# Kernel tuning notes

Hardware: AMD Instinct MI355X
Metric: run time of the kernel (lower is better)

The kernel has to match this reference:

```python
import jax, jax.numpy as jnp
import numpy as np

# Physical constants and grid (match torch WRF.__init__)
PREF = 100000.0
RD = 287.0
G = 9.81
NX, NY, NZ = 384, 384, 48
DX, DY = 1000.0, 1000.0
DZ = 1.0 / (NZ + 1)

# --- staggered-grid stencil primitives (replace F.conv3d with shifts) ---

def pad_x(X):
    # periodic in x
    return jnp.concatenate([X[:, :, -1:], X, X[:, :, :1]], axis=2)

def pad_y(X):
    # periodic in y
    return jnp.concatenate([X[:, -1:, :], X, X[:, :1, :]], axis=1)

def pad_z(X, top=None, surface=None):
    # Dirichlet in z (defaults to zero boundary planes)
    top = top if top is not None else jnp.zeros_like(X[:1])
    surface = surface if surface is not None else jnp.zeros_like(X[:1])
    return jnp.concatenate([top, X, surface], axis=0)

def bar_x(X):
    return (X[:, :, 1:] + X[:, :, :-1]) * 0.5

def bar_y(X):
    return (X[:, 1:, :] + X[:, :-1, :]) * 0.5

def bar_z(X):
    return (X[1:] + X[:-1]) * 0.5

def delta_x(X):
    return (X[:, :, 1:] - X[:, :, :-1]) / DX

def delta_y(X):
    return (X[:, 1:, :] - X[:, :-1, :]) / DY

def delta_z(X):
    return (X[1:] - X[:-1]) / DZ


def rhs(U, V, W, Theta, Mu, Phi, Phi_t, Phi_s, P_t, P_s):
    u = U / bar_x(pad_x(Mu))                      # (NZ, NY, NX+1)
    v = V / bar_y(pad_y(Mu))                      # (NZ, NY+1, NX)
    w = W / bar_z(Mu)                             # (NZ-1, NY, NX)
    alpha = -delta_z(pad_z(Phi, Phi_t, Phi_s)) / Mu   # (NZ, NY, NX)
    theta = Theta / Mu
    p = PREF * (RD * theta / PREF / alpha) ** 1.4
    omega = -w * G / bar_z(alpha) / bar_z(Mu)     # (NZ-1, NY, NX)
    Omega = omega * bar_z(Mu)

    R_U = (-delta_x(bar_x(pad_x(U)) * bar_x(pad_x(u)))
           - delta_y(bar_x(pad_x(V)) * bar_y(pad_y(u)))
           - delta_z(bar_x(pad_x(pad_z(Omega))) * bar_z(pad_z(u))))
    R_V = (-delta_x(bar_y(pad_y(U)) * bar_x(pad_x(v)))
           - delta_y(bar_y(pad_y(V)) * bar_y(pad_y(v)))
           - delta_z(bar_y(pad_y(pad_z(Omega))) * bar_z(pad_z(v))))
    R_W = (-delta_x(bar_z(U) * bar_x(pad_x(w)))
           - delta_y(bar_z(V) * bar_y(pad_y(w)))
           - delta_z(bar_z(pad_z(Omega)) * bar_z(pad_z(w))))
    R_Theta = (-delta_x(U * bar_x(pad_x(theta)))
               - delta_y(V * bar_y(pad_y(theta)))
               - delta_z(pad_z(Omega) * bar_z(pad_z(theta))))
    R_Phi = (-bar_z(bar_x(u)) * delta_x(bar_x(pad_x(Phi)))
             - bar_z(bar_y(v)) * delta_y(bar_y(pad_y(Phi)))
             - omega * delta_z(bar_z(pad_z(Phi, Phi_t, Phi_s))))
    R_Mu = -delta_x(U) - delta_y(V) - delta_z(pad_z(Omega))

    # pressure-gradient terms
    R_U = R_U + (-bar_x(pad_x(Mu)) * bar_x(pad_x(alpha)) * delta_x(pad_x(p))
                 - delta_z(bar_x(bar_z(pad_x(pad_z(p, P_t, P_s)))))
                   * delta_x(pad_x(bar_z(pad_z(Phi, Phi_t, Phi_s)))))
    R_V = R_V + (-bar_y(pad_y(Mu)) * bar_y(pad_y(alpha)) * delta_y(pad_y(p))
                 - delta_z(bar_y(bar_z(pad_y(pad_z(p, P_t, P_s)))))
                   * delta_y(pad_y(bar_z(pad_z(Phi, Phi_t, Phi_s)))))
    R_W = R_W + G * (delta_z(p) - bar_z(Mu))
    R_Phi = R_Phi + G * w
    return R_U, R_V, R_W, R_Theta, R_Mu, R_Phi


def rk3_step(U, V, W, Theta, Mu, Phi, Phi_t, Phi_s, P_t, P_s, dt):
    Uc, Vc, Wc, Tc, Mc, Pc = U, V, W, Theta, Mu, Phi
    for c in (dt / 3.0, dt / 2.0, dt * 1.0):
        rU, rV, rW, rT, rM, rP = rhs(Uc, Vc, Wc, Tc, Mc, Pc, Phi_t, Phi_s, P_t, P_s)
        Uc = U + c * rU
        Vc = V + c * rV
        Wc = W + c * rW
        Tc = Theta + c * rT
        Mc = Mu + c * rM
        Pc = Phi + c * rP
    return (Uc, Vc, Wc, Tc, Mc, Pc)


def setup_inputs() -> dict:
    key = jax.random.key(0)
    k_th, k_u, k_v, k_w = jax.random.split(key, 4)
    # potential temperature with boundary layers, ~300 K
    theta_full = 300.0 + 0.5 * jax.random.normal(k_th, (NZ + 2, NY, NX), dtype=jnp.float32)
    P_t = jnp.zeros((1, NY, NX), dtype=jnp.float32)
    P_s = jnp.full((1, NY, NX), PREF, dtype=jnp.float32)
    # reproduce __init__ hydrostatic setup
    P = jnp.linspace(DZ, 1.0 - DZ, NZ, dtype=jnp.float32).reshape(NZ, 1, 1) * (P_s - P_t) + P_t
    Alpha = RD / PREF * theta_full[1:-1] * (P / PREF) ** (-1.0 / 1.4)
    Mu = jnp.broadcast_to(P_s - P_t, (NZ, NY, NX)).astype(jnp.float32)
    layer = Mu * Alpha * DZ                                  # (NZ, NY, NX)
    # Phi_full[i] = sum_{j>=i} layer[j], Phi_full[NZ] = 0
    Phi_full = jnp.concatenate(
        [jnp.flip(jnp.cumsum(jnp.flip(layer, 0), axis=0), 0),
         jnp.zeros((1, NY, NX), dtype=jnp.float32)], axis=0)  # (NZ+1, NY, NX)
    Phi_t = Phi_full[:1]
    Phi_s = Phi_full[-1:]
    Phi = Phi_full[1:-1]                                     # (NZ-1, NY, NX)
    Theta = theta_full[1:-1] * Mu
    U = 5e5 * jax.random.normal(k_u, (NZ, NY, NX + 1), dtype=jnp.float32)
    V = 5e5 * jax.random.normal(k_v, (NZ, NY + 1, NX), dtype=jnp.float32)
    W = 1e4 * jax.random.normal(k_w, (NZ - 1, NY, NX), dtype=jnp.float32)
    return {"U": U, "V": V, "W": W, "Theta": Theta, "Mu": Mu, "Phi": Phi,
            "Phi_t": Phi_t, "Phi_s": Phi_s, "P_t": P_t, "P_s": P_s, "dt": 4}


def reference(U, V, W, Theta, Mu, Phi, Phi_t, Phi_s, P_t, P_s, dt):
    return rk3_step(U, V, W, Theta, Mu, Phi, Phi_t, Phi_s, P_t, P_s, dt)
```

## Files before the change

kernel.cpp:

```cpp
#include <hip/hip_runtime.h>

namespace {

constexpr int NX = 384, NY = 384, NZ = 48;
constexpr int NXU = NX + 1;
constexpr int PLN = NX * NY;
constexpr float RDX = 1.0f / 1000.0f;
constexpr float RDY = 1.0f / 1000.0f;
constexpr float RDZ = 49.0f;
constexpr float PREF = 100000.0f, G = 9.81f;
constexpr float K_RP = 287.0f / PREF;

constexpr int SZ_U = NZ * NY * NXU;
constexpr int SZ_V = NZ * (NY + 1) * NX;
constexpr int SZ_W = (NZ - 1) * PLN;
constexpr int SZ_T = NZ * PLN;
constexpr int SZ_M = NZ * PLN;
constexpr int SZ_P = (NZ - 1) * PLN;

constexpr int TX = 32, TY = 8;
constexpr int PW = TX + 3;
constexpr int PH = TY + 3;
constexpr int PSZ = PW * PH;
constexpr int WW = PW + 1;
constexpr int WH = PH + 1;
constexpr int WSZ = WW * WH;
constexpr int ZP = 448;
constexpr int KCH = 12, KSPLIT = 4;

constexpr int GX = NX / TX;
constexpr int GY = NY / TY;
constexpr int NWG = GX * GY * KSPLIT;
constexpr int CPX = NWG / 8;

constexpr int O_PH = 0;
constexpr int O_MS = O_PH + 5 * ZP;
constexpr int O_UR = O_MS + 4 * ZP;
constexpr int O_VR = O_UR + 3 * ZP;
constexpr int O_TS = O_VR + 3 * ZP;
constexpr int O_WS = O_TS + ZP;
constexpr int O_P  = O_WS + ZP;
constexpr int O_OM = O_P  + 3 * PSZ;
constexpr int O_TH = O_OM + 3 * PSZ;
constexpr int O_u  = O_TH + 2 * PSZ;
constexpr int O_v  = O_u  + 2 * PSZ;
constexpr int O_w  = O_v  + 2 * PSZ;
constexpr int LTOT = O_w + 2 * PSZ;

struct PIdx { int pix, uo, vo, wc, oxa, oxb, oya, oyb; };

__device__ __forceinline__ float frcp(float x) { return __builtin_amdgcn_rcpf(x); }
__device__ __forceinline__ float pow14(float x) {
    return __builtin_amdgcn_exp2f(1.4f * __builtin_amdgcn_logf(x));
}
__device__ __forceinline__ void gll4(const float* src, float* ldsWaveBase) {
    __builtin_amdgcn_global_load_lds(
        (const __attribute__((address_space(1))) void*)src,
        (__attribute__((address_space(3))) void*)ldsWaveBase, 4, 0, 0);
}
__device__ __forceinline__ int imin(int a, int b) { return a < b ? a : b; }
__device__ __forceinline__ int imax(int a, int b) { return a > b ? a : b; }

__global__ __launch_bounds__(256, 3)
void rhs_tile(
    const float* __restrict__ Us, const float* __restrict__ Vs, const float* __restrict__ Ws,
    const float* __restrict__ Ts, const float* __restrict__ Ms, const float* __restrict__ Ps,
    const float* __restrict__ Phit, const float* __restrict__ Phis,
    const float* __restrict__ Pt,   const float* __restrict__ Psrf,
    const float* __restrict__ U0, const float* __restrict__ V0, const float* __restrict__ W0,
    const float* __restrict__ T0, const float* __restrict__ M0, const float* __restrict__ P0,
    float* __restrict__ Uo, float* __restrict__ Vo, float* __restrict__ Wo,
    float* __restrict__ To, float* __restrict__ Mo, float* __restrict__ Po,
    const int* __restrict__ dtp, float coef)
{
    __shared__ float L[LTOT];

    const int tx = threadIdx.x, ty = threadIdx.y;
    const int tid = ty * TX + tx;

    const int flat = blockIdx.x + GX * (blockIdx.y + GY * blockIdx.z);
    const int nf   = (flat & 7) * CPX + (flat >> 3);
    const int bx   = nf % GX;
    const int by   = (nf / GX) % GY;
    const int bz   = nf / (GX * GY);
    const int i0 = bx * TX;
    const int j0 = by * TY;
    const int k0 = bz * KCH;

    const int i = i0 + tx, j = j0 + ty;
    const float c = coef * (float)(*dtp);
    const int ly = ty + 1, lx = tx + 1;
    const int wb = tid & ~63;
    const bool w2 = (tid < 192);
    const bool hasB = (tid + 256 < PSZ);
    const bool hasW = (tid + 256 < WSZ);

    auto mkpt = [&](int idx, PIdx& q) {
        const int r = idx / PW, cc = idx - r * PW;
        int gj = j0 - 1 + r;  if (gj < 0) gj += NY; else if (gj >= NY) gj -= NY;
        int gi = i0 - 1 + cc; if (gi < 0) gi += NX; else if (gi >= NX) gi -= NX;
        int gII = i0 - 1 + cc; if (gII < 0) gII += NX + 1; else if (gII > NX) gII -= NX + 1;
        int gJJ = j0 - 1 + r;  if (gJJ < 0) gJJ += NY + 1; else if (gJJ > NY) gJJ -= NY + 1;
        q.pix = gj * NX + gi;
        q.uo  = gj * NXU + gII;
        q.vo  = gJJ * NX + gi;
        q.wc  = (r + 1) * WW + (cc + 1);
        q.oxa = q.wc - 1; q.oxb = q.wc;
        if (i0 == 0 && cc == 0) { q.oxa = q.wc; q.oxb = q.wc + 1; }
        q.oya = q.wc - WW; q.oyb = q.wc;
        if (j0 == 0 && r == 0)  { q.oya = q.wc; q.oyb = q.wc + WW; }
    };
    auto mkwide = [&](int idxw) -> int {
        const int r = idxw / WW, cc = idxw - r * WW;
        int gj = j0 - 2 + r;  if (gj < 0) gj += NY; else if (gj >= NY) gj -= NY;
        int gi = i0 - 2 + cc; if (gi < 0) gi += NX; else if (gi >= NX) gi -= NX;
        return gj * NX + gi;
    };
    PIdx A, B;
    mkpt(tid, A);
    mkpt(imin(tid + 256, PSZ - 1), B);
    const int pwA = mkwide(tid);
    const int pwB = mkwide(imin(tid + 256, WSZ - 1));

    auto stage = [&](int k) {
        {
            const int m = k + 3;
            const float* sA = (m >= NZ - 1) ? &Phis[A.pix] : &Ps[m * PLN + A.pix];
            gll4(sA, &L[O_PH + (m % 5) * ZP + wb]);
            if (w2) {
                const float* sB = (m >= NZ - 1) ? &Phis[B.pix] : &Ps[m * PLN + B.pix];
                gll4(sB, &L[O_PH + (m % 5) * ZP + wb + 256]);
            }
        }
        {
            const int lm = imin(k + 3, NZ - 1);
            gll4(&Ms[lm * PLN + pwA], &L[O_MS + ((k + 3) % 4) * ZP + wb]);
            if (w2) gll4(&Ms[lm * PLN + pwB], &L[O_MS + ((k + 3) % 4) * ZP + wb + 256]);
        }
        {
            const int lc = imin(k + 2, NZ - 1);
            gll4(&Us[lc * NY * NXU + A.uo], &L[O_UR + ((k + 2) % 3) * ZP + wb]);
            if (w2) gll4(&Us[lc * NY * NXU + B.uo], &L[O_UR + ((k + 2) % 3) * ZP + wb + 256]);
            gll4(&Vs[lc * (NY + 1) * NX + A.vo], &L[O_VR + ((k + 2) % 3) * ZP + wb]);
            if (w2) gll4(&Vs[lc * (NY + 1) * NX + B.vo], &L[O_VR + ((k + 2) % 3) * ZP + wb + 256]);
            gll4(&Ts[lc * PLN + A.pix], &L[O_TS + wb]);
            if (w2) gll4(&Ts[lc * PLN + B.pix], &L[O_TS + wb + 256]);
            const int lw = imin(k + 2, NZ - 2);
            gll4(&Ws[lw * PLN + A.pix], &L[O_WS + wb]);
            if (w2) gll4(&Ws[lw * PLN + B.pix], &L[O_WS + wb + 256]);
        }
    };

    auto derive = [&](int l, int idx, const PIdx& q, float tsv, float wsv) {
        const int s3 = ((l % 3) + 3) % 3, s2 = l & 1;
        float pv, th = 0.f, uv = 0.f, vv = 0.f, wv = 0.f, om = 0.f;
        if (l >= 0 && l < NZ) {
            const int m4 = l % 4, m5 = l % 5, p5 = ((l - 1) % 5 + 5) % 5;
            const float mu  = L[O_MS + m4 * ZP + q.wc];
            const float phv = L[O_PH + m5 * ZP + idx];
            const float phm = L[O_PH + p5 * ZP + idx];
            const float rmu = frcp(mu);
            const float al  = -(phv - phm) * RDZ * rmu;
            th = tsv * rmu;
            pv = PREF * pow14(K_RP * th * frcp(al));
            uv = L[O_UR + (l % 3) * ZP + idx]
                 * frcp(0.5f * (L[O_MS + m4 * ZP + q.oxa] + L[O_MS + m4 * ZP + q.oxb]));
            vv = L[O_VR + (l % 3) * ZP + idx]
                 * frcp(0.5f * (L[O_MS + m4 * ZP + q.oya] + L[O_MS + m4 * ZP + q.oyb]));
            if (l < NZ - 1) {
                const float mu1 = L[O_MS + ((l + 1) % 4) * ZP + q.wc];
                const float ph1 = L[O_PH + ((l + 1) % 5) * ZP + idx];
                const float al1 = -(ph1 - phv) * RDZ * frcp(mu1);
                const float mz  = 0.5f * (mu + mu1);
                wv = wsv * frcp(mz);
                om = -wsv * G * frcp(0.5f * (al + al1) * mz);
            }
        } else {
            pv = (l < 0) ? Pt[q.pix] : Psrf[q.pix];
        }
        L[O_P  + s3 * PSZ + idx] = pv;
        L[O_OM + s3 * PSZ + idx] = om;
        L[O_TH + s2 * PSZ + idx] = th;
        L[O_u  + s2 * PSZ + idx] = uv;
        L[O_v  + s2 * PSZ + idx] = vv;
        L[O_w  + s2 * PSZ + idx] = wv;
    };

    {
        for (int m = k0 - 2; m <= k0 + 2; ++m) {
            const float v = (m >= NZ - 1) ? Phis[A.pix]
                          : ((m < 0) ? Phit[A.pix] : Ps[m * PLN + A.pix]);
            L[O_PH + ((m % 5 + 5) % 5) * ZP + tid] = v;
        }
        for (int l = k0 - 1; l <= k0 + 2; ++l) {
            const int lc = imin(imax(l, 0), NZ - 1);
            L[O_MS + ((l % 4 + 4) % 4) * ZP + tid] = Ms[lc * PLN + pwA];
        }
        for (int l = k0 - 1; l <= k0 + 1; ++l) {
            const int lc = imin(imax(l, 0), NZ - 1);
            L[O_UR + ((l % 3 + 3) % 3) * ZP + tid] = Us[lc * NY * NXU + A.uo];
            L[O_VR + ((l % 3 + 3) % 3) * ZP + tid] = Vs[lc * (NY + 1) * NX + A.vo];
        }
        if (hasB) {
            const int idx = tid + 256;
            for (int m = k0 - 2; m <= k0 + 2; ++m) {
                const float v = (m >= NZ - 1) ? Phis[B.pix]
                              : ((m < 0) ? Phit[B.pix] : Ps[m * PLN + B.pix]);
                L[O_PH + ((m % 5 + 5) % 5) * ZP + idx] = v;
            }
            for (int l = k0 - 1; l <= k0 + 1; ++l) {
                const int lc = imin(imax(l, 0), NZ - 1);
                L[O_UR + ((l % 3 + 3) % 3) * ZP + idx] = Us[lc * NY * NXU + B.uo];
                L[O_VR + ((l % 3 + 3) % 3) * ZP + idx] = Vs[lc * (NY + 1) * NX + B.vo];
            }
        }
        if (hasW) {
            const int idx = tid + 256;
            for (int l = k0 - 1; l <= k0 + 2; ++l) {
                const int lc = imin(imax(l, 0), NZ - 1);
                L[O_MS + ((l % 4 + 4) % 4) * ZP + idx] = Ms[lc * PLN + pwB];
            }
        }
    }
    __syncthreads();

    {
        int lc = imin(imax(k0 - 1, 0), NZ - 1), lw = imin(imax(k0 - 1, 0), NZ - 2);
        derive(k0 - 1, tid, A, Ts[lc * PLN + A.pix], Ws[lw * PLN + A.pix]);
        if (hasB) derive(k0 - 1, tid + 256, B, Ts[lc * PLN + B.pix], Ws[lw * PLN + B.pix]);
        lc = imin(k0, NZ - 1); lw = imin(k0, NZ - 2);
        derive(k0, tid, A, Ts[lc * PLN + A.pix], Ws[lw * PLN + A.pix]);
        if (hasB) derive(k0, tid + 256, B, Ts[lc * PLN + B.pix], Ws[lw * PLN + B.pix]);
    }
    {
        const int lc = imin(k0 + 1, NZ - 1), lw = imin(k0 + 1, NZ - 2);
        gll4(&Ts[lc * PLN + A.pix], &L[O_TS + wb]);
        if (w2) gll4(&Ts[lc * PLN + B.pix], &L[O_TS + wb + 256]);
        gll4(&Ws[lw * PLN + A.pix], &L[O_WS + wb]);
        if (w2) gll4(&Ws[lw * PLN + B.pix], &L[O_WS + wb + 256]);
    }
    __syncthreads();

    const int e0 = (k0 - 1) & 1;
    float th_m  = L[O_TH + e0 * PSZ + ly * PW + lx];
    float u_m   = L[O_u  + e0 * PSZ + ly * PW + lx];
    float u_m_e = L[O_u  + e0 * PSZ + ly * PW + lx + 1];
    float v_m   = L[O_v  + e0 * PSZ + ly * PW + lx];
    float v_m_e = L[O_v  + e0 * PSZ + (ly + 1) * PW + lx];
    float w_m   = L[O_w  + e0 * PSZ + ly * PW + lx];

    for (int k = k0; k < k0 + KCH; ++k) {
        derive(k + 1, tid, A, L[O_TS + tid], L[O_WS + tid]);
        if (hasB) derive(k + 1, tid + 256, B, L[O_TS + tid + 256], L[O_WS + tid + 256]);
        __syncthreads();

        if (k < k0 + KCH - 1) stage(k);

        const int a5 = (k + 4) % 5, b5 = k % 5, c5 = (k + 1) % 5;
        const int aP = (k + 2) % 3, bP = k % 3, cP = (k + 1) % 3;
        const int m4 = k % 4, n4 = (k + 1) % 4;
        const int e = k & 1, f = 1 - e;
        const int eU = k % 3, fU = (k + 1) % 3;

        auto PHx = [&](int s, int rr, int cc) { return L[O_PH + s * ZP + rr * PW + cc]; };
        auto Px  = [&](int s, int rr, int cc) { return L[O_P  + s * PSZ + rr * PW + cc]; };
        auto Ox  = [&](int s, int rr, int cc) { return L[O_OM + s * PSZ + rr * PW + cc]; };
        auto MUx = [&](int s, int rr, int cc) { return L[O_MS + s * ZP + (rr + 1) * WW + cc + 1]; };
        auto THx = [&](int s, int rr, int cc) { return L[O_TH + s * PSZ + rr * PW + cc]; };
        auto URx = [&](int s, int rr, int cc) { return L[O_UR + s * ZP + rr * PW + cc]; };
        auto VRx = [&](int s, int rr, int cc) { return L[O_VR + s * ZP + rr * PW + cc]; };
        auto ux  = [&](int s, int rr, int cc) { return L[O_u  + s * PSZ + rr * PW + cc]; };
        auto vx  = [&](int s, int rr, int cc) { return L[O_v  + s * PSZ + rr * PW + cc]; };
        auto wx  = [&](int s, int rr, int cc) { return L[O_w  + s * PSZ + rr * PW + cc]; };
        auto ALk = [&](int rr, int cc) {
            return -(PHx(b5, rr, cc) - PHx(a5, rr, cc)) * RDZ * frcp(MUx(m4, rr, cc));
        };

        auto R_U_c = [&](int cc, float ukm) -> float {
            const float u0 = ux(e, ly, cc), um = ux(e, ly, cc - 1), up = ux(e, ly, cc + 1);
            const float Uc = URx(eU, ly, cc), Um = URx(eU, ly, cc - 1), Up = URx(eU, ly, cc + 1);
            float r = -0.25f * ((Uc + Up) * (u0 + up) - (Um + Uc) * (um + u0)) * RDX;
            const float VBj  = 0.5f * (VRx(eU, ly, cc - 1) + VRx(eU, ly, cc));
            const float VBj1 = 0.5f * (VRx(eU, ly + 1, cc - 1) + VRx(eU, ly + 1, cc));
            const float uS = ux(e, ly - 1, cc), uN = ux(e, ly + 1, cc);
            r -= (VBj1 * 0.5f * (u0 + uN) - VBj * 0.5f * (uS + u0)) * RDY;
            const float OBk  = 0.5f * (Ox(aP, ly, cc - 1) + Ox(aP, ly, cc));
            const float OBk1 = 0.5f * (Ox(bP, ly, cc - 1) + Ox(bP, ly, cc));
            const float ukp = ux(f, ly, cc);
            r -= (OBk1 * 0.5f * (u0 + ukp) - OBk * 0.5f * (ukm + u0)) * RDZ;
            const float mux_ = 0.5f * (MUx(m4, ly, cc - 1) + MUx(m4, ly, cc));
            const float alx  = 0.5f * (ALk(ly, cc - 1) + ALk(ly, cc));
            const float dpx  = (Px(bP, ly, cc) - Px(bP, ly, cc - 1)) * RDX;
            r -= mux_ * alx * dpx;
            const float pzk  = 0.25f * (Px(aP, ly, cc - 1) + Px(bP, ly, cc - 1)
                                      + Px(aP, ly, cc)     + Px(bP, ly, cc));
            const float pzk1 = 0.25f * (Px(bP, ly, cc - 1) + Px(cP, ly, cc - 1)
                                      + Px(bP, ly, cc)     + Px(cP, ly, cc));
            const float dpz = (pzk1 - pzk) * RDZ;
            const float pza = 0.5f * (PHx(a5, ly, cc - 1) + PHx(b5, ly, cc - 1));
            const float pzb = 0.5f * (PHx(a5, ly, cc)     + PHx(b5, ly, cc));
            r -= dpz * (pzb - pza) * RDX;
            return r;
        };

        auto R_V_c = [&](int rr, float vkm) -> float {
            const float v0 = vx(e, rr, lx), vm = vx(e, rr - 1, lx), vp = vx(e, rr + 1, lx);
            const float Vc = VRx(eU, rr, lx), Vm = VRx(eU, rr - 1, lx), Vp = VRx(eU, rr + 1, lx);
            float r = -0.25f * ((Vc + Vp) * (v0 + vp) - (Vm + Vc) * (vm + v0)) * RDY;
            const float UBi  = 0.5f * (URx(eU, rr - 1, lx)     + URx(eU, rr, lx));
            const float UBi1 = 0.5f * (URx(eU, rr - 1, lx + 1) + URx(eU, rr, lx + 1));
            const float vW = vx(e, rr, lx - 1), vE = vx(e, rr, lx + 1);
            r -= (UBi1 * 0.5f * (v0 + vE) - UBi * 0.5f * (vW + v0)) * RDX;
            const float OBk  = 0.5f * (Ox(aP, rr - 1, lx) + Ox(aP, rr, lx));
            const float OBk1 = 0.5f * (Ox(bP, rr - 1, lx) + Ox(bP, rr, lx));
            const float vkp = vx(f, rr, lx);
            r -= (OBk1 * 0.5f * (v0 + vkp) - OBk * 0.5f * (vkm + v0)) * RDZ;
            const float muy = 0.5f * (MUx(m4, rr - 1, lx) + MUx(m4, rr, lx));
            const float aly = 0.5f * (ALk(rr - 1, lx) + ALk(rr, lx));
            const float dpy = (Px(bP, rr, lx) - Px(bP, rr - 1, lx)) * RDY;
            r -= muy * aly * dpy;
            const float pzk  = 0.25f * (Px(aP, rr - 1, lx) + Px(bP, rr - 1, lx)
                                      + Px(aP, rr, lx)     + Px(bP, rr, lx));
            const float pzk1 = 0.25f * (Px(bP, rr - 1, lx) + Px(cP, rr - 1, lx)
                                      + Px(bP, rr, lx)     + Px(cP, rr, lx));
            const float dpz = (pzk1 - pzk) * RDZ;
            const float pza = 0.5f * (PHx(a5, rr - 1, lx) + PHx(b5, rr - 1, lx));
            const float pzb = 0.5f * (PHx(a5, rr, lx)     + PHx(b5, rr, lx));
            r -= dpz * (pzb - pza) * RDY;
            return r;
        };

        const float th0 = THx(e, ly, lx);
        float rT = -(URx(eU, ly, lx + 1) * 0.5f * (th0 + THx(e, ly, lx + 1))
                   - URx(eU, ly, lx)     * 0.5f * (THx(e, ly, lx - 1) + th0)) * RDX
                   -(VRx(eU, ly + 1, lx) * 0.5f * (th0 + THx(e, ly + 1, lx))
                   - VRx(eU, ly, lx)     * 0.5f * (THx(e, ly - 1, lx) + th0)) * RDY;
        const float th_p = THx(f, ly, lx);
        const float Hk  = Ox(aP, ly, lx) * 0.5f * (th_m + th0);
        const float Hk1 = Ox(bP, ly, lx) * 0.5f * (th0 + th_p);
        rT -= (Hk1 - Hk) * RDZ;

        const float rM = -(URx(eU, ly, lx + 1) - URx(eU, ly, lx)) * RDX
                         -(VRx(eU, ly + 1, lx) - VRx(eU, ly, lx)) * RDY
                         -(Ox(bP, ly, lx) - Ox(aP, ly, lx)) * RDZ;

        const int idc = (k * NY + j) * NX + i;
        To[idc] = T0[idc] + c * rT;
        Mo[idc] = M0[idc] + c * rM;
        const int idu = (k * NY + j) * NXU + i;
        Uo[idu] = U0[idu] + c * R_U_c(lx, u_m);
        const int idv = (k * (NY + 1) + j) * NX + i;
        Vo[idv] = V0[idv] + c * R_V_c(ly, v_m);

        if (k < NZ - 1) {
            const float w0 = wx(e, ly, lx);
            const float Uzi  = 0.5f * (URx(eU, ly, lx)     + URx(fU, ly, lx));
            const float Uzi1 = 0.5f * (URx(eU, ly, lx + 1) + URx(fU, ly, lx + 1));
            const float wW = wx(e, ly, lx - 1), wE = wx(e, ly, lx + 1);
            float rW = -(Uzi1 * 0.5f * (w0 + wE) - Uzi * 0.5f * (wW + w0)) * RDX;
            const float Vzj  = 0.5f * (VRx(eU, ly, lx)     + VRx(fU, ly, lx));
            const float Vzj1 = 0.5f * (VRx(eU, ly + 1, lx) + VRx(fU, ly + 1, lx));
            const float wS = wx(e, ly - 1, lx), wN = wx(e, ly + 1, lx);
            rW -= (Vzj1 * 0.5f * (w0 + wN) - Vzj * 0.5f * (wS + w0)) * RDY;
            const float OZk  = 0.5f * (Ox(aP, ly, lx) + Ox(bP, ly, lx));
            const float OZk1 = 0.5f * (Ox(bP, ly, lx) + Ox(cP, ly, lx));
            const float wkp = wx(f, ly, lx);
            rW -= (OZk1 * 0.5f * (w0 + wkp) - OZk * 0.5f * (w_m + w0)) * RDZ;
            const float muz = 0.5f * (MUx(m4, ly, lx) + MUx(n4, ly, lx));
            rW += G * ((Px(cP, ly, lx) - Px(bP, ly, lx)) * RDZ - muz);

            const float ubz = 0.25f * (ux(e, ly, lx) + ux(e, ly, lx + 1)
                                     + ux(f, ly, lx) + ux(f, ly, lx + 1));
            const float dfx = (PHx(b5, ly, lx + 1) - PHx(b5, ly, lx - 1)) * (0.5f * RDX);
            const float vbz = 0.25f * (vx(e, ly, lx) + vx(e, ly + 1, lx)
                                     + vx(f, ly, lx) + vx(f, ly + 1, lx));
            const float dfy = (PHx(b5, ly + 1, lx) - PHx(b5, ly - 1, lx)) * (0.5f * RDY);
            const float rmuz = frcp(muz);
            const float om   = Ox(bP, ly, lx) * rmuz;
            const float dfz  = (PHx(c5, ly, lx) - PHx(a5, ly, lx)) * (0.5f * RDZ);
            const float rP = -ubz * dfx - vbz * dfy - om * dfz + G * w0;

            Wo[idc] = W0[idc] + c * rW;
            Po[idc] = P0[idc] + c * rP;
        }

        if (i == NX - 1) {
            Uo[idu + 1] = U0[idu + 1] + c * R_U_c(lx + 1, u_m_e);
        }
        if (j == NY - 1) {
            const int idv2 = (k * (NY + 1) + NY) * NX + i;
            Vo[idv2] = V0[idv2] + c * R_V_c(ly + 1, v_m_e);
        }

        th_m  = th0;
        u_m   = ux(e, ly, lx);
        u_m_e = ux(e, ly, lx + 1);
        v_m   = vx(e, ly, lx);
        v_m_e = vx(e, ly + 1, lx);
        w_m   = wx(e, ly, lx);

        __syncthreads();
    }
}

}

extern "C" void kernel_launch(void* const* d_in, const int* in_sizes, int n_in,
                              void* d_out, int out_size, void* d_ws, size_t ws_size,
                              hipStream_t stream)
{
    (void)in_sizes; (void)n_in; (void)out_size; (void)ws_size;

    const float* U0   = (const float*)d_in[0];
    const float* V0   = (const float*)d_in[1];
    const float* W0   = (const float*)d_in[2];
    const float* T0   = (const float*)d_in[3];
    const float* M0   = (const float*)d_in[4];
    const float* P0   = (const float*)d_in[5];
    const float* Phit = (const float*)d_in[6];
    const float* Phis = (const float*)d_in[7];
    const float* Pt   = (const float*)d_in[8];
    const float* Psrf = (const float*)d_in[9];
    const int*   dtp  = (const int*)d_in[10];

    float* out = (float*)d_out;
    float* ws  = (float*)d_ws;

    float* outU = out;
    float* outV = outU + SZ_U;
    float* outW = outV + SZ_V;
    float* outT = outW + SZ_W;
    float* outM = outT + SZ_T;
    float* outP = outM + SZ_M;

    float* wsU = ws;
    float* wsV = wsU + SZ_U;
    float* wsW = wsV + SZ_V;
    float* wsT = wsW + SZ_W;
    float* wsM = wsT + SZ_T;
    float* wsP = wsM + SZ_M;

    const dim3 blk(TX, TY, 1);
    const dim3 grd(GX, GY, KSPLIT);

    const float coefs[3] = {1.0f / 3.0f, 0.5f, 1.0f};

    const float* sU[3] = {U0, outU, wsU};
    const float* sV[3] = {V0, outV, wsV};
    const float* sW[3] = {W0, outW, wsW};
    const float* sT[3] = {T0, outT, wsT};
    const float* sM[3] = {M0, outM, wsM};
    const float* sP_[3] = {P0, outP, wsP};
    float* oU[3] = {outU, wsU, outU};
    float* oV[3] = {outV, wsV, outV};
    float* oW[3] = {outW, wsW, outW};
    float* oT[3] = {outT, wsT, outT};
    float* oM[3] = {outM, wsM, outM};
    float* oP[3] = {outP, wsP, outP};

    for (int s = 0; s < 3; ++s) {
        rhs_tile<<<grd, blk, 0, stream>>>(
            sU[s], sV[s], sW[s], sT[s], sM[s], sP_[s],
            Phit, Phis, Pt, Psrf,
            U0, V0, W0, T0, M0, P0,
            oU[s], oV[s], oW[s], oT[s], oM[s], oP[s],
            dtp, coefs[s]);
    }
}
```

Baseline: 539.6 us.

## Drop LDS rings for U/V/T/W, recompute mass fluxes from u*mu, raise occupancy

Removes the shared-memory ring buffers for the raw U, V, Theta and W fields. These values are now prefetched into registers with ordinary global loads, and the flux values U and V are rebuilt in the stencil as velocity times the averaged Mu. The Phi and Mu rings are resized to their exact tile sizes, with scalar tail stores covering the part the async loads do not fill. The smaller LDS footprint lets launch bounds go from 3 to 4 blocks per CU. The cost is extra multiplies and LDS reads for the rebuilt fluxes, more register pressure, and rounding that may differ slightly from the loaded U and V.

Result: slower. 1.498 ms (+177.5%).

```diff
diff --git a/kernel.cpp b/kernel.cpp
--- a/kernel.cpp
+++ b/kernel.cpp
@@ -25,7 +25,6 @@
 constexpr int WW = PW + 1;
 constexpr int WH = PH + 1;
 constexpr int WSZ = WW * WH;
-constexpr int ZP = 448;
 constexpr int KCH = 12, KSPLIT = 4;
 
 constexpr int GX = NX / TX;
@@ -34,12 +33,8 @@
 constexpr int CPX = NWG / 8;
 
 constexpr int O_PH = 0;
-constexpr int O_MS = O_PH + 5 * ZP;
-constexpr int O_UR = O_MS + 4 * ZP;
-constexpr int O_VR = O_UR + 3 * ZP;
-constexpr int O_TS = O_VR + 3 * ZP;
-constexpr int O_WS = O_TS + ZP;
-constexpr int O_P  = O_WS + ZP;
+constexpr int O_MS = O_PH + 5 * PSZ;
+constexpr int O_P  = O_MS + 4 * WSZ;
 constexpr int O_OM = O_P  + 3 * PSZ;
 constexpr int O_TH = O_OM + 3 * PSZ;
 constexpr int O_u  = O_TH + 2 * PSZ;
@@ -61,7 +56,7 @@
 __device__ __forceinline__ int imin(int a, int b) { return a < b ? a : b; }
 __device__ __forceinline__ int imax(int a, int b) { return a > b ? a : b; }
 
-__global__ __launch_bounds__(256, 3)
+__global__ __launch_bounds__(256, 4)
 void rhs_tile(
     const float* __restrict__ Us, const float* __restrict__ Vs, const float* __restrict__ Ws,
     const float* __restrict__ Ts, const float* __restrict__ Ms, const float* __restrict__ Ps,
@@ -91,7 +86,6 @@
     const float c = coef * (float)(*dtp);
     const int ly = ty + 1, lx = tx + 1;
     const int wb = tid & ~63;
-    const bool w2 = (tid < 192);
     const bool hasB = (tid + 256 < PSZ);
     const bool hasW = (tid + 256 < WSZ);
 
@@ -122,54 +116,54 @@
     const int pwA = mkwide(tid);
     const int pwB = mkwide(imin(tid + 256, WSZ - 1));
 
+    const int msT = tid - 128;
+    const bool hasMsT = (msT >= 0 && msT < WSZ - 384);
+    const int pwT = mkwide(hasMsT ? (384 + msT) : 0);
+    int p384;
+    { PIdx tq; mkpt(PSZ - 1, tq); p384 = tq.pix; }
+    const bool hasPhT = (tid == 176);
+
     auto stage = [&](int k) {
-        {
-            const int m = k + 3;
-            const float* sA = (m >= NZ - 1) ? &Phis[A.pix] : &Ps[m * PLN + A.pix];
-            gll4(sA, &L[O_PH + (m % 5) * ZP + wb]);
-            if (w2) {
-                const float* sB = (m >= NZ - 1) ? &Phis[B.pix] : &Ps[m * PLN + B.pix];
-                gll4(sB, &L[O_PH + (m % 5) * ZP + wb + 256]);
-            }
-        }
-        {
-            const int lm = imin(k + 3, NZ - 1);
-            gll4(&Ms[lm * PLN + pwA], &L[O_MS + ((k + 3) % 4) * ZP + wb]);
-            if (w2) gll4(&Ms[lm * PLN + pwB], &L[O_MS + ((k + 3) % 4) * ZP + wb + 256]);
-        }
-        {
-            const int lc = imin(k + 2, NZ - 1);
-            gll4(&Us[lc * NY * NXU + A.uo], &L[O_UR + ((k + 2) % 3) * ZP + wb]);
-            if (w2) gll4(&Us[lc * NY * NXU + B.uo], &L[O_UR + ((k + 2) % 3) * ZP + wb + 256]);
-            gll4(&Vs[lc * (NY + 1) * NX + A.vo], &L[O_VR + ((k + 2) % 3) * ZP + wb]);
-            if (w2) gll4(&Vs[lc * (NY + 1) * NX + B.vo], &L[O_VR + ((k + 2) % 3) * ZP + wb + 256]);
-            gll4(&Ts[lc * PLN + A.pix], &L[O_TS + wb]);
-            if (w2) gll4(&Ts[lc * PLN + B.pix], &L[O_TS + wb + 256]);
-            const int lw = imin(k + 2, NZ - 2);
-            gll4(&Ws[lw * PLN + A.pix], &L[O_WS + wb]);
-            if (w2) gll4(&Ws[lw * PLN + B.pix], &L[O_WS + wb + 256]);
-        }
+        const int m = k + 3;
+        const float* sA = (m >= NZ - 1) ? &Phis[A.pix] : &Ps[m * PLN + A.pix];
+        gll4(sA, &L[O_PH + (m % 5) * PSZ + wb]);
+        if (tid < 128) {
+            const float* sB = (m >= NZ - 1) ? &Phis[B.pix] : &Ps[m * PLN + B.pix];
+            gll4(sB, &L[O_PH + (m % 5) * PSZ + wb + 256]);
+        }
+        const int lm = imin(m, NZ - 1);
+        gll4(&Ms[lm * PLN + pwA], &L[O_MS + (m % 4) * WSZ + wb]);
+        if (tid < 128) gll4(&Ms[lm * PLN + pwB], &L[O_MS + (m % 4) * WSZ + wb + 256]);
     };
-
-    auto derive = [&](int l, int idx, const PIdx& q, float tsv, float wsv) {
+    auto stage_tail = [&](int k) {
+        const int m = k + 3;
+        if (hasPhT) {
+            L[O_PH + (m % 5) * PSZ + (PSZ - 1)] =
+                (m >= NZ - 1) ? Phis[p384] : Ps[m * PLN + p384];
+        }
+        if (hasMsT) {
+            const int lm = imin(m, NZ - 1);
+            L[O_MS + (m % 4) * WSZ + 384 + msT] = Ms[lm * PLN + pwT];
+        }
+    };
+
+    auto derive = [&](int l, int idx, const PIdx& q, float Uv, float Vv, float tsv, float wsv) {
         const int s3 = ((l % 3) + 3) % 3, s2 = l & 1;
         float pv, th = 0.f, uv = 0.f, vv = 0.f, wv = 0.f, om = 0.f;
         if (l >= 0 && l < NZ) {
             const int m4 = l % 4, m5 = l % 5, p5 = ((l - 1) % 5 + 5) % 5;
-            const float mu  = L[O_MS + m4 * ZP + q.wc];
-            const float phv = L[O_PH + m5 * ZP + idx];
-            const float phm = L[O_PH + p5 * ZP + idx];
+            const float mu  = L[O_MS + m4 * WSZ + q.wc];
+            const float phv = L[O_PH + m5 * PSZ + idx];
+            const float phm = L[O_PH + p5 * PSZ + idx];
             const float rmu = frcp(mu);
             const float al  = -(phv - phm) * RDZ * rmu;
             th = tsv * rmu;
             pv = PREF * pow14(K_RP * th * frcp(al));
-            uv = L[O_UR + (l % 3) * ZP + idx]
-                 * frcp(0.5f * (L[O_MS + m4 * ZP + q.oxa] + L[O_MS + m4 * ZP + q.oxb]));
-            vv = L[O_VR + (l % 3) * ZP + idx]
-                 * frcp(0.5f * (L[O_MS + m4 * ZP + q.oya] + L[O_MS + m4 * ZP + q.oyb]));
+            uv = Uv * frcp(0.5f * (L[O_MS + m4 * WSZ + q.oxa] + L[O_MS + m4 * WSZ + q.oxb]));
+            vv = Vv * frcp(0.5f * (L[O_MS + m4 * WSZ + q.oya] + L[O_MS + m4 * WSZ + q.oyb]));
             if (l < NZ - 1) {
-                const float mu1 = L[O_MS + ((l + 1) % 4) * ZP + q.wc];
-                const float ph1 = L[O_PH + ((l + 1) % 5) * ZP + idx];
+                const float mu1 = L[O_MS + ((l + 1) % 4) * WSZ + q.wc];
+                const float ph1 = L[O_PH + ((l + 1) % 5) * PSZ + idx];
                 const float al1 = -(ph1 - phv) * RDZ * frcp(mu1);
                 const float mz  = 0.5f * (mu + mu1);
                 wv = wsv * frcp(mz);
@@ -190,35 +184,25 @@
         for (int m = k0 - 2; m <= k0 + 2; ++m) {
             const float v = (m >= NZ - 1) ? Phis[A.pix]
                           : ((m < 0) ? Phit[A.pix] : Ps[m * PLN + A.pix]);
-            L[O_PH + ((m % 5 + 5) % 5) * ZP + tid] = v;
+            L[O_PH + ((m % 5 + 5) % 5) * PSZ + tid] = v;
         }
         for (int l = k0 - 1; l <= k0 + 2; ++l) {
             const int lc = imin(imax(l, 0), NZ - 1);
-            L[O_MS + ((l % 4 + 4) % 4) * ZP + tid] = Ms[lc * PLN + pwA];
-        }
-        for (int l = k0 - 1; l <= k0 + 1; ++l) {
-            const int lc = imin(imax(l, 0), NZ - 1);
-            L[O_UR + ((l % 3 + 3) % 3) * ZP + tid] = Us[lc * NY * NXU + A.uo];
-            L[O_VR + ((l % 3 + 3) % 3) * ZP + tid] = Vs[lc * (NY + 1) * NX + A.vo];
+            L[O_MS + ((l % 4 + 4) % 4) * WSZ + tid] = Ms[lc * PLN + pwA];
         }
         if (hasB) {
             const int idx = tid + 256;
             for (int m = k0 - 2; m <= k0 + 2; ++m) {
                 const float v = (m >= NZ - 1) ? Phis[B.pix]
                               : ((m < 0) ? Phit[B.pix] : Ps[m * PLN + B.pix]);
-                L[O_PH + ((m % 5 + 5) % 5) * ZP + idx] = v;
-            }
-            for (int l = k0 - 1; l <= k0 + 1; ++l) {
-                const int lc = imin(imax(l, 0), NZ - 1);
-                L[O_UR + ((l % 3 + 3) % 3) * ZP + idx] = Us[lc * NY * NXU + B.uo];
-                L[O_VR + ((l % 3 + 3) % 3) * ZP + idx] = Vs[lc * (NY + 1) * NX + B.vo];
+                L[O_PH + ((m % 5 + 5) % 5) * PSZ + idx] = v;
             }
         }
         if (hasW) {
             const int idx = tid + 256;
             for (int l = k0 - 1; l <= k0 + 2; ++l) {
                 const int lc = imin(imax(l, 0), NZ - 1);
-                L[O_MS + ((l % 4 + 4) % 4) * ZP + idx] = Ms[lc * PLN + pwB];
+                L[O_MS + ((l % 4 + 4) % 4) * WSZ + idx] = Ms[lc * PLN + pwB];
             }
         }
     }
@@ -226,18 +210,26 @@
 
     {
         int lc = imin(imax(k0 - 1, 0), NZ - 1), lw = imin(imax(k0 - 1, 0), NZ - 2);
-        derive(k0 - 1, tid, A, Ts[lc * PLN + A.pix], Ws[lw * PLN + A.pix]);
-        if (hasB) derive(k0 - 1, tid + 256, B, Ts[lc * PLN + B.pix], Ws[lw * PLN + B.pix]);
+        derive(k0 - 1, tid, A, Us[lc * NY * NXU + A.uo], Vs[lc * (NY + 1) * NX + A.vo],
+               Ts[lc * PLN + A.pix], Ws[lw * PLN + A.pix]);
+        if (hasB) derive(k0 - 1, tid + 256, B, Us[lc * NY * NXU + B.uo],
+                         Vs[lc * (NY + 1) * NX + B.vo], Ts[lc * PLN + B.pix], Ws[lw * PLN + B.pix]);
         lc = imin(k0, NZ - 1); lw = imin(k0, NZ - 2);
-        derive(k0, tid, A, Ts[lc * PLN + A.pix], Ws[lw * PLN + A.pix]);
-        if (hasB) derive(k0, tid + 256, B, Ts[lc * PLN + B.pix], Ws[lw * PLN + B.pix]);
+        derive(k0, tid, A, Us[lc * NY * NXU + A.uo], Vs[lc * (NY + 1) * NX + A.vo],
+               Ts[lc * PLN + A.pix], Ws[lw * PLN + A.pix]);
+        if (hasB) derive(k0, tid + 256, B, Us[lc * NY * NXU + B.uo],
+                         Vs[lc * (NY + 1) * NX + B.vo], Ts[lc * PLN + B.pix], Ws[lw * PLN + B.pix]);
     }
+
+    float cUa, cVa, cTa, cWa, cUb = 0.f, cVb = 0.f, cTb = 0.f, cWb = 0.f;
     {
         const int lc = imin(k0 + 1, NZ - 1), lw = imin(k0 + 1, NZ - 2);
-        gll4(&Ts[lc * PLN + A.pix], &L[O_TS + wb]);
-        if (w2) gll4(&Ts[lc * PLN + B.pix], &L[O_TS + wb + 256]);
-        gll4(&Ws[lw * PLN + A.pix], &L[O_WS + wb]);
-        if (w2) gll4(&Ws[lw * PLN + B.pix], &L[O_WS + wb + 256]);
+        cUa = Us[lc * NY * NXU + A.uo]; cVa = Vs[lc * (NY + 1) * NX + A.vo];
+        cTa = Ts[lc * PLN + A.pix];     cWa = Ws[lw * PLN + A.pix];
+        if (hasB) {
+            cUb = Us[lc * NY * NXU + B.uo]; cVb = Vs[lc * (NY + 1) * NX + B.vo];
+            cTb = Ts[lc * PLN + B.pix];     cWb = Ws[lw * PLN + B.pix];
+        }
     }
     __syncthreads();
 
@@ -250,45 +242,65 @@
     float w_m   = L[O_w  + e0 * PSZ + ly * PW + lx];
 
     for (int k = k0; k < k0 + KCH; ++k) {
-        derive(k + 1, tid, A, L[O_TS + tid], L[O_WS + tid]);
-        if (hasB) derive(k + 1, tid + 256, B, L[O_TS + tid + 256], L[O_WS + tid + 256]);
+        derive(k + 1, tid, A, cUa, cVa, cTa, cWa);
+        if (hasB) derive(k + 1, tid + 256, B, cUb, cVb, cTb, cWb);
         __syncthreads();
 
-        if (k < k0 + KCH - 1) stage(k);
+        if (k < k0 + KCH - 1) {
+            stage(k);
+            stage_tail(k);
+            const int lc = imin(k + 2, NZ - 1), lw = imin(k + 2, NZ - 2);
+            cUa = Us[lc * NY * NXU + A.uo]; cVa = Vs[lc * (NY + 1) * NX + A.vo];
+            cTa = Ts[lc * PLN + A.pix];     cWa = Ws[lw * PLN + A.pix];
+            if (hasB) {
+                cUb = Us[lc * NY * NXU + B.uo]; cVb = Vs[lc * (NY + 1) * NX + B.vo];
+                cTb = Ts[lc * PLN + B.pix];     cWb = Ws[lw * PLN + B.pix];
+            }
+        }
 
         const int a5 = (k + 4) % 5, b5 = k % 5, c5 = (k + 1) % 5;
         const int aP = (k + 2) % 3, bP = k % 3, cP = (k + 1) % 3;
         const int m4 = k % 4, n4 = (k + 1) % 4;
         const int e = k & 1, f = 1 - e;
-        const int eU = k % 3, fU = (k + 1) % 3;
-
-        auto PHx = [&](int s, int rr, int cc) { return L[O_PH + s * ZP + rr * PW + cc]; };
+
+        auto PHx = [&](int s, int rr, int cc) { return L[O_PH + s * PSZ + rr * PW + cc]; };
         auto Px  = [&](int s, int rr, int cc) { return L[O_P  + s * PSZ + rr * PW + cc]; };
         auto Ox  = [&](int s, int rr, int cc) { return L[O_OM + s * PSZ + rr * PW + cc]; };
-        auto MUx = [&](int s, int rr, int cc) { return L[O_MS + s * ZP + (rr + 1) * WW + cc + 1]; };
+        auto MSW = [&](int s, int widx)       { return L[O_MS + s * WSZ + widx]; };
+        auto MUx = [&](int s, int rr, int cc) { return MSW(s, (rr + 1) * WW + cc + 1); };
         auto THx = [&](int s, int rr, int cc) { return L[O_TH + s * PSZ + rr * PW + cc]; };
-        auto URx = [&](int s, int rr, int cc) { return L[O_UR + s * ZP + rr * PW + cc]; };
-        auto VRx = [&](int s, int rr, int cc) { return L[O_VR + s * ZP + rr * PW + cc]; };
         auto ux  = [&](int s, int rr, int cc) { return L[O_u  + s * PSZ + rr * PW + cc]; };
         auto vx  = [&](int s, int rr, int cc) { return L[O_v  + s * PSZ + rr * PW + cc]; };
         auto wx  = [&](int s, int rr, int cc) { return L[O_w  + s * PSZ + rr * PW + cc]; };
+        auto MUXP = [&](int s, int rr, int cc) {
+            const int wc = (rr + 1) * WW + cc + 1;
+            const bool sm = (i0 == 0) && (cc == 0);
+            return 0.5f * (MSW(s, sm ? wc : wc - 1) + MSW(s, sm ? wc + 1 : wc));
+        };
+        auto MUYP = [&](int s, int rr, int cc) {
+            const int wc = (rr + 1) * WW + cc + 1;
+            const bool sm = (j0 == 0) && (rr == 0);
+            return 0.5f * (MSW(s, sm ? wc : wc - WW) + MSW(s, sm ? wc + WW : wc));
+        };
+        auto Ur = [&](int s2, int s4, int rr, int cc) { return ux(s2, rr, cc) * MUXP(s4, rr, cc); };
+        auto Vr = [&](int s2, int s4, int rr, int cc) { return vx(s2, rr, cc) * MUYP(s4, rr, cc); };
         auto ALk = [&](int rr, int cc) {
             return -(PHx(b5, rr, cc) - PHx(a5, rr, cc)) * RDZ * frcp(MUx(m4, rr, cc));
         };
 
         auto R_U_c = [&](int cc, float ukm) -> float {
             const float u0 = ux(e, ly, cc), um = ux(e, ly, cc - 1), up = ux(e, ly, cc + 1);
-            const float Uc = URx(eU, ly, cc), Um = URx(eU, ly, cc - 1), Up = URx(eU, ly, cc + 1);
+            const float Uc = Ur(e, m4, ly, cc), Um = Ur(e, m4, ly, cc - 1), Up = Ur(e, m4, ly, cc + 1);
             float r = -0.25f * ((Uc + Up) * (u0 + up) - (Um + Uc) * (um + u0)) * RDX;
-            const float VBj  = 0.5f * (VRx(eU, ly, cc - 1) + VRx(eU, ly, cc));
-            const float VBj1 = 0.5f * (VRx(eU, ly + 1, cc - 1) + VRx(eU, ly + 1, cc));
+            const float VBj  = 0.5f * (Vr(e, m4, ly, cc - 1) + Vr(e, m4, ly, cc));
+            const float VBj1 = 0.5f * (Vr(e, m4, ly + 1, cc - 1) + Vr(e, m4, ly + 1, cc));
             const float uS = ux(e, ly - 1, cc), uN = ux(e, ly + 1, cc);
             r -= (VBj1 * 0.5f * (u0 + uN) - VBj * 0.5f * (uS + u0)) * RDY;
             const float OBk  = 0.5f * (Ox(aP, ly, cc - 1) + Ox(aP, ly, cc));
             const float OBk1 = 0.5f * (Ox(bP, ly, cc - 1) + Ox(bP, ly, cc));
             const float ukp = ux(f, ly, cc);
             r -= (OBk1 * 0.5f * (u0 + ukp) - OBk * 0.5f * (ukm + u0)) * RDZ;
-            const float mux_ = 0.5f * (MUx(m4, ly, cc - 1) + MUx(m4, ly, cc));
+            const float mux_ = MUXP(m4, ly, cc);
             const float alx  = 0.5f * (ALk(ly, cc - 1) + ALk(ly, cc));
             const float dpx  = (Px(bP, ly, cc) - Px(bP, ly, cc - 1)) * RDX;
             r -= mux_ * alx * dpx;
@@ -305,17 +317,17 @@
 
         auto R_V_c = [&](int rr, float vkm) -> float {
             const float v0 = vx(e, rr, lx), vm = vx(e, rr - 1, lx), vp = vx(e, rr + 1, lx);
-            const float Vc = VRx(eU, rr, lx), Vm = VRx(eU, rr - 1, lx), Vp = VRx(eU, rr + 1, lx);
+            const float Vc = Vr(e, m4, rr, lx), Vm = Vr(e, m4, rr - 1, lx), Vp = Vr(e, m4, rr + 1, lx);
             float r = -0.25f * ((Vc + Vp) * (v0 + vp) - (Vm + Vc) * (vm + v0)) * RDY;
-            const float UBi  = 0.5f * (URx(eU, rr - 1, lx)     + URx(eU, rr, lx));
-            const float UBi1 = 0.5f * (URx(eU, rr - 1, lx + 1) + URx(eU, rr, lx + 1));
+            const float UBi  = 0.5f * (Ur(e, m4, rr - 1, lx)     + Ur(e, m4, rr, lx));
+            const float UBi1 = 0.5f * (Ur(e, m4, rr - 1, lx + 1) + Ur(e, m4, rr, lx + 1));
             const float vW = vx(e, rr, lx - 1), vE = vx(e, rr, lx + 1);
             r -= (UBi1 * 0.5f * (v0 + vE) - UBi * 0.5f * (vW + v0)) * RDX;
             const float OBk  = 0.5f * (Ox(aP, rr - 1, lx) + Ox(aP, rr, lx));
             const float OBk1 = 0.5f * (Ox(bP, rr - 1, lx) + Ox(bP, rr, lx));
             const float vkp = vx(f, rr, lx);
             r -= (OBk1 * 0.5f * (v0 + vkp) - OBk * 0.5f * (vkm + v0)) * RDZ;
-            const float muy = 0.5f * (MUx(m4, rr - 1, lx) + MUx(m4, rr, lx));
+            const float muy = MUYP(m4, rr, lx);
             const float aly = 0.5f * (ALk(rr - 1, lx) + ALk(rr, lx));
             const float dpy = (Px(bP, rr, lx) - Px(bP, rr - 1, lx)) * RDY;
             r -= muy * aly * dpy;
@@ -331,17 +343,17 @@
         };
 
         const float th0 = THx(e, ly, lx);
-        float rT = -(URx(eU, ly, lx + 1) * 0.5f * (th0 + THx(e, ly, lx + 1))
-                   - URx(eU, ly, lx)     * 0.5f * (THx(e, ly, lx - 1) + th0)) * RDX
-                   -(VRx(eU, ly + 1, lx) * 0.5f * (th0 + THx(e, ly + 1, lx))
-                   - VRx(eU, ly, lx)     * 0.5f * (THx(e, ly - 1, lx) + th0)) * RDY;
+        float rT = -(Ur(e, m4, ly, lx + 1) * 0.5f * (th0 + THx(e, ly, lx + 1))
+                   - Ur(e, m4, ly, lx)     * 0.5f * (THx(e, ly, lx - 1) + th0)) * RDX
+                   -(Vr(e, m4, ly + 1, lx) * 0.5f * (th0 + THx(e, ly + 1, lx))
+                   - Vr(e, m4, ly, lx)     * 0.5f * (THx(e, ly - 1, lx) + th0)) * RDY;
         const float th_p = THx(f, ly, lx);
         const float Hk  = Ox(aP, ly, lx) * 0.5f * (th_m + th0);
         const float Hk1 = Ox(bP, ly, lx) * 0.5f * (th0 + th_p);
         rT -= (Hk1 - Hk) * RDZ;
 
-        const float rM = -(URx(eU, ly, lx + 1) - URx(eU, ly, lx)) * RDX
-                         -(VRx(eU, ly + 1, lx) - VRx(eU, ly, lx)) * RDY
+        const float rM = -(Ur(e, m4, ly, lx + 1) - Ur(e, m4, ly, lx)) * RDX
+                         -(Vr(e, m4, ly + 1, lx) - Vr(e, m4, ly, lx)) * RDY
                          -(Ox(bP, ly, lx) - Ox(aP, ly, lx)) * RDZ;
 
         const int idc = (k * NY + j) * NX + i;
@@ -354,12 +366,12 @@
 
         if (k < NZ - 1) {
             const float w0 = wx(e, ly, lx);
-            const float Uzi  = 0.5f * (URx(eU, ly, lx)     + URx(fU, ly, lx));
-            const float Uzi1 = 0.5f * (URx(eU, ly, lx + 1) + URx(fU, ly, lx + 1));
+            const float Uzi  = 0.5f * (Ur(e, m4, ly, lx)     + Ur(f, n4, ly, lx));
+            const float Uzi1 = 0.5f * (Ur(e, m4, ly, lx + 1) + Ur(f, n4, ly, lx + 1));
             const float wW = wx(e, ly, lx - 1), wE = wx(e, ly, lx + 1);
             float rW = -(Uzi1 * 0.5f * (w0 + wE) - Uzi * 0.5f * (wW + w0)) * RDX;
-            const float Vzj  = 0.5f * (VRx(eU, ly, lx)     + VRx(fU, ly, lx));
-            const float Vzj1 = 0.5f * (VRx(eU, ly + 1, lx) + VRx(fU, ly + 1, lx));
+            const float Vzj  = 0.5f * (Vr(e, m4, ly, lx)     + Vr(f, n4, ly, lx));
+            const float Vzj1 = 0.5f * (Vr(e, m4, ly + 1, lx) + Vr(f, n4, ly + 1, lx));
             const float wS = wx(e, ly - 1, lx), wN = wx(e, ly + 1, lx);
             rW -= (Vzj1 * 0.5f * (w0 + wN) - Vzj * 0.5f * (wS + w0)) * RDY;
             const float OZk  = 0.5f * (Ox(aP, ly, lx) + Ox(bP, ly, lx));
```
